# Optimization experiments

Measured on AMD Instinct MI355X. Metric: run time of the kernel, lower is better.

## Reference

```python
import jax, jax.numpy as jnp
import numpy as np

T, D = 4096, 2048
H, DK, DV = 6, 256, 512        # heads, head_k_dim, head_v_dim (expand_v=2)
KD, VD = H * DK, H * DV        # 1536, 3072
KSZ = 4                        # conv_size
GEN = D // 8                   # generator reduction 8 -> 256
EPS = 1e-5                     # norm_eps


def setup_inputs() -> dict:
    key = jax.random.key(0)
    ks = jax.random.split(key, 12)
    std = 0.02
    p = lambda i, shape: jax.random.normal(ks[i], shape, jnp.float32) * std
    rng = np.random.default_rng(0)
    A = rng.uniform(0.0, 16.0, H).astype(np.float32)
    dt = np.exp(rng.uniform(0, 1, H) * (np.log(0.1) - np.log(0.001)) + np.log(0.001)).astype(np.float32)
    dt = np.clip(dt, 1e-4, None)
    inv_dt = (dt + np.log(-np.expm1(-dt))).astype(np.float32)
    return {
        'hidden_states': jax.random.normal(ks[0], (T, D), jnp.float32),
        'Wq': p(1, (D, KD)), 'Wk': p(2, (D, KD)), 'Wv': p(3, (D, VD)),
        'Wb': p(4, (D, H)), 'Wa': p(5, (D, H)), 'Wg': p(6, (D, VD)), 'Wo': p(7, (VD, D)),
        'A_log': jnp.asarray(np.log(A)), 'dt_bias': jnp.asarray(inv_dt),
        'conv_w': p(8, (VD, KSZ)), 'gen_w1': p(9, (D, GEN)), 'gen_w2': p(10, (GEN, KSZ)),
        'norm_w': jnp.ones((DV,), jnp.float32),
    }


def _l2norm(x):
    return x * jax.lax.rsqrt(jnp.sum(x * x, -1, keepdims=True) + 1e-6)


def reference(hidden_states, Wq, Wk, Wv, Wb, Wa, Wg, Wo, A_log, dt_bias, conv_w, gen_w1, gen_w2, norm_w):
    h = hidden_states[None]                             # [1,T,D]
    q = jax.nn.silu(h @ Wq)                             # [1,T,KD]
    k = jax.nn.silu(h @ Wk)
    x = h @ Wv                                          # [1,T,VD]
    # dynamic short convolution: per-token kernel added to static depthwise kernel
    dyn = jax.nn.silu(h @ gen_w1) @ gen_w2              # [1,T,KSZ]
    xpad = jnp.pad(x, ((0, 0), (KSZ - 1, 0), (0, 0)))   # causal padding
    v = jnp.zeros_like(x)
    for j in range(KSZ):
        v = v + (conv_w[None, None, :, j] + dyn[:, :, None, j]) * xpad[:, j:j + x.shape[1], :]
    v = jax.nn.silu(v)

    B = 1
    q = _l2norm(q.reshape(B, -1, H, DK))                # use_qk_l2norm_in_kernel=True
    k = _l2norm(k.reshape(B, -1, H, DK))
    v = v.reshape(B, -1, H, DV)
    beta = jax.nn.sigmoid(h @ Wb)                       # [1,T,H]
    g = -jnp.exp(A_log) * jax.nn.softplus(h @ Wa + dt_bias)  # [1,T,H] decay log-gates
    scale = DK ** -0.5

    def step(S, inp):                                   # gated delta rule recurrence
        qt, kt, vt, gt, bt = inp
        S = S * jnp.exp(gt)[..., None, None]            # [B,H,DK,DV]
        dv = (vt - jnp.einsum('bhk,bhkv->bhv', kt, S)) * bt[..., None]
        S = S + kt[..., :, None] * dv[..., None, :]
        ot = jnp.einsum('bhk,bhkv->bhv', qt, S) * scale
        return S, ot

    S0 = jnp.zeros((B, H, DK, DV), jnp.float32)
    tm = lambda a: jnp.moveaxis(a, 1, 0)                # time-major for scan
    _, o = jax.lax.scan(step, S0, (tm(q), tm(k), tm(v), tm(g), tm(beta)))
    o = jnp.moveaxis(o, 0, 1)                           # [1,T,H,DV]

    gate = (h @ Wg).reshape(B, -1, H, DV)
    rms = jax.lax.rsqrt(jnp.mean(o * o, -1, keepdims=True) + EPS)
    o = o * rms * norm_w * jax.nn.silu(gate)            # gated RMSNorm
    o = o.reshape(B, -1, VD) @ Wo                       # [1,T,D]
    return o[0]
```

## Files before the change

kernel.cpp:

```cpp
#include <hip/hip_runtime.h>
#include <hip/hip_bf16.h>
#include <math.h>

#define T_LEN 4096
#define DIM   2048
#define NH    6
#define DK    256
#define DVh   512
#define KD    1536
#define VD    3072
#define CK    64
#define NCHK  (T_LEN / CK)
#define NFUSE 9472

typedef __attribute__((ext_vector_type(8))) short bf16x8;
typedef __attribute__((ext_vector_type(4))) float f32x4;

#define AS1 __attribute__((address_space(1)))
#define AS3 __attribute__((address_space(3)))

__device__ __forceinline__ float silu_f(float v){ return v / (1.f + __expf(-v)); }

__device__ __forceinline__ unsigned short f2bf(float f) {
  unsigned int u = __float_as_uint(f);
  unsigned int r = u + 0x7FFFu + ((u >> 16) & 1u);
  return (unsigned short)(r >> 16);
}
__device__ __forceinline__ float bf2f(unsigned short s) {
  return __uint_as_float(((unsigned int)s) << 16);
}

__device__ __forceinline__ void bar_lds() {
  __builtin_amdgcn_sched_barrier(0);
  asm volatile("s_waitcnt lgkmcnt(0)" ::: "memory");
  __builtin_amdgcn_s_barrier();
  __builtin_amdgcn_sched_barrier(0);
}

__global__ __launch_bounds__(256) void cast_bf16(
    const float* __restrict__ in, unsigned short* __restrict__ out)
{
  int i = blockIdx.x * 256 + threadIdx.x;
  float4 v4 = ((const float4*)in)[i];
  ushort4 o4;
  o4.x = f2bf(v4.x); o4.y = f2bf(v4.y); o4.z = f2bf(v4.z); o4.w = f2bf(v4.w);
  ((ushort4*)out)[i] = o4;
}

__global__ __launch_bounds__(256) void tcast_all(
    const float* __restrict__ Wq, const float* __restrict__ Wk,
    const float* __restrict__ Wv, const float* __restrict__ Wg,
    const float* __restrict__ g1, const float* __restrict__ Wo,
    unsigned short* __restrict__ wTall, unsigned short* __restrict__ wT)
{
  int id = blockIdx.x;
  const float* in; unsigned short* out; int R, Cn, nbx;
  if (id < 3072)       { in = Wq; out = wTall;                          R = 2048; Cn = 1536; nbx = 48; }
  else if (id < 6144)  { in = Wk; out = wTall + (size_t)1536 * 2048;    R = 2048; Cn = 1536; nbx = 48; id -= 3072; }
  else if (id < 12288) { in = Wv; out = wTall + (size_t)3072 * 2048;    R = 2048; Cn = 3072; nbx = 96; id -= 6144; }
  else if (id < 18432) { in = Wg; out = wTall + (size_t)6144 * 2048;    R = 2048; Cn = 3072; nbx = 96; id -= 12288; }
  else if (id < 18944) { in = g1; out = wTall + (size_t)9216 * 2048;    R = 2048; Cn = 256;  nbx = 8;  id -= 18432; }
  else                 { in = Wo; out = wT;                             R = 3072; Cn = 2048; nbx = 64; id -= 18944; }
  int bx = (id % nbx) * 32, by = (id / nbx) * 32;
  __shared__ float tile[32][33];
  int tx = threadIdx.x & 31, ty = threadIdx.x >> 5;
#pragma unroll
  for (int i = 0; i < 32; i += 8)
    tile[ty + i][tx] = in[(size_t)(by + ty + i) * Cn + bx + tx];
  __syncthreads();
#pragma unroll
  for (int i = 0; i < 32; i += 8)
    out[(size_t)(bx + ty + i) * R + by + tx] = f2bf(tile[tx][ty + i]);
}

#define PSTAGE(Amat, Bmat, bufi, t_, Aptr, Bptr, Kk) do { \
    int k0_ = (t_) << 6; \
    _Pragma("unroll") \
    for (int i_ = 0; i_ < 4; ++i_) { \
      int c_ = threadIdx.x + 256 * i_; \
      int ks_ = c_ >> 9, row_ = (c_ >> 2) & 127, pc_ = c_ & 3; \
      int pcs_ = pc_ ^ ((row_ >> 1) & 3); \
      int gc_ = k0_ + ks_ * 32 + pcs_ * 8; \
      __builtin_amdgcn_global_load_lds( \
          (const AS1 unsigned int*)(Aptr + (size_t)(bm + row_) * (Kk) + gc_), \
          (AS3 unsigned int*)(&Amat[bufi][0] + c_ * 8), 16, 0, 0); \
      __builtin_amdgcn_global_load_lds( \
          (const AS1 unsigned int*)(Bptr + (size_t)(bn + row_) * (Kk) + gc_), \
          (AS3 unsigned int*)(&Bmat[bufi][0] + c_ * 8), 16, 0, 0); \
    } } while (0)

#define PGEMM_LOOP(Amat, Bmat, Aptr, Bptr, Kk, NTt) do { \
    PSTAGE(Amat, Bmat, 0, 0, Aptr, Bptr, Kk); \
    PSTAGE(Amat, Bmat, 1, 1, Aptr, Bptr, Kk); \
    __builtin_amdgcn_sched_barrier(0); \
    asm volatile("s_waitcnt vmcnt(8)" ::: "memory"); \
    __builtin_amdgcn_s_barrier(); \
    __builtin_amdgcn_sched_barrier(0); \
    const int slot_ = (kq ^ ((fr >> 1) & 3)) * 8; \
    for (int t = 0; t < (NTt); ++t) { \
      const unsigned short* as_ = &Amat[t & 1][0]; \
      const unsigned short* bs_ = &Bmat[t & 1][0]; \
      bf16x8 af_[2][4], bf_[2][4]; \
      _Pragma("unroll") \
      for (int ks_ = 0; ks_ < 2; ++ks_) { \
        _Pragma("unroll") \
        for (int i_ = 0; i_ < 4; ++i_) { \
          af_[ks_][i_] = *(const bf16x8*)(as_ + ks_ * 4096 + (wm + i_ * 16 + fr) * 32 + slot_); \
          bf_[ks_][i_] = *(const bf16x8*)(bs_ + ks_ * 4096 + (wn + i_ * 16 + fr) * 32 + slot_); \
        } } \
      __builtin_amdgcn_s_setprio(1); \
      _Pragma("unroll") \
      for (int i_ = 0; i_ < 4; ++i_) \
        _Pragma("unroll") \
        for (int j_ = 0; j_ < 4; ++j_) \
          acc[i_][j_] = __builtin_amdgcn_mfma_f32_16x16x32_bf16(af_[0][i_], bf_[0][j_], acc[i_][j_], 0, 0, 0); \
      __builtin_amdgcn_s_setprio(0); \
      bar_lds(); \
      if (t + 2 < (NTt)) PSTAGE(Amat, Bmat, t & 1, t + 2, Aptr, Bptr, Kk); \
      __builtin_amdgcn_s_setprio(1); \
      _Pragma("unroll") \
      for (int i_ = 0; i_ < 4; ++i_) \
        _Pragma("unroll") \
        for (int j_ = 0; j_ < 4; ++j_) \
          acc[i_][j_] = __builtin_amdgcn_mfma_f32_16x16x32_bf16(af_[1][i_], bf_[1][j_], acc[i_][j_], 0, 0, 0); \
      __builtin_amdgcn_s_setprio(0); \
      __builtin_amdgcn_sched_barrier(0); \
      if (t + 2 < (NTt)) { asm volatile("s_waitcnt vmcnt(8)" ::: "memory"); } \
      else               { asm volatile("s_waitcnt vmcnt(0)" ::: "memory"); } \
      __builtin_amdgcn_s_barrier(); \
      __builtin_amdgcn_sched_barrier(0); \
    } } while (0)

__global__ __launch_bounds__(256) void gemm_bt_bf16(
    const unsigned short* __restrict__ A, const unsigned short* __restrict__ BT,
    void* __restrict__ Cout, int M, int N, int K, int act)
{
  __shared__ unsigned short As[2][8192];
  __shared__ unsigned short Bs[2][8192];
  const int tid = threadIdx.x;
  const int bm = blockIdx.y * 128, bn = blockIdx.x * 128;
  const int lane = tid & 63, wave = tid >> 6;
  const int wm = (wave >> 1) * 64, wn = (wave & 1) * 64;
  const int fr = lane & 15, kq = lane >> 4;
  const int NT = K >> 6;

  f32x4 acc[4][4];
#pragma unroll
  for (int i = 0; i < 4; ++i)
#pragma unroll
    for (int j = 0; j < 4; ++j) acc[i][j] = (f32x4){0.f, 0.f, 0.f, 0.f};

  PGEMM_LOOP(As, Bs, A, BT, K, NT);

  if (act == 2) {
    unsigned short* C = (unsigned short*)Cout;
#pragma unroll
    for (int i = 0; i < 4; ++i) {
      int rbase = bm + wm + i * 16 + kq * 4;
#pragma unroll
      for (int r = 0; r < 4; ++r) {
        size_t rowoff = (size_t)(rbase + r) * N + bn + wn + fr;
#pragma unroll
        for (int j = 0; j < 4; ++j) C[rowoff + j * 16] = f2bf(acc[i][j][r]);
      }
    }
  } else {
    float* C = (float*)Cout;
#pragma unroll
    for (int i = 0; i < 4; ++i) {
      int rbase = bm + wm + i * 16 + kq * 4;
#pragma unroll
      for (int r = 0; r < 4; ++r) {
        size_t rowoff = (size_t)(rbase + r) * N + bn + wn + fr;
#pragma unroll
        for (int j = 0; j < 4; ++j) {
          float v = acc[i][j][r];
          if (act == 1) v = silu_f(v);
          C[rowoff + j * 16] = v;
        }
      }
    }
  }
}

__global__ __launch_bounds__(256) void gemm_fused(
    const unsigned short* __restrict__ A, const unsigned short* __restrict__ BT,
    float* __restrict__ Cq, float* __restrict__ Ck, float* __restrict__ Cx,
    unsigned short* __restrict__ Cg, float* __restrict__ Ct)
{
  __shared__ unsigned short As[2][8192];
  __shared__ unsigned short Bs[2][8192];
  const int tid = threadIdx.x;
  const int NPN = NFUSE / 128;
  const int GROUP = 8;
  const int npig = GROUP * NPN;
  const int pid = blockIdx.x;
  const int gid = pid / npig;
  const int pm = gid * GROUP + (pid % GROUP);
  const int pn = (pid % npig) / GROUP;
  const int bm = pm * 128, bn = pn * 128;
  const int lane = tid & 63, wave = tid >> 6;
  const int wm = (wave >> 1) * 64, wn = (wave & 1) * 64;
  const int fr = lane & 15, kq = lane >> 4;
  const int NT = DIM >> 6;

  f32x4 acc[4][4];
#pragma unroll
  for (int i = 0; i < 4; ++i)
#pragma unroll
    for (int j = 0; j < 4; ++j) acc[i][j] = (f32x4){0.f, 0.f, 0.f, 0.f};

  PGEMM_LOOP(As, Bs, A, BT, DIM, NT);

  float* Fd = nullptr; unsigned short* Bd = nullptr;
  int strideN, cb, mode;
  if (bn < 1536)      { Fd = Cq; strideN = 1536; cb = bn;        mode = 1; }
  else if (bn < 3072) { Fd = Ck; strideN = 1536; cb = bn - 1536; mode = 1; }
  else if (bn < 6144) { Fd = Cx; strideN = 3072; cb = bn - 3072; mode = 0; }
  else if (bn < 9216) { Bd = Cg; strideN = 3072; cb = bn - 6144; mode = 2; }
  else                { Fd = Ct; strideN = 256;  cb = bn - 9216; mode = 1; }

  if (mode == 2) {
#pragma unroll
    for (int i = 0; i < 4; ++i) {
      int rbase = bm + wm + i * 16 + kq * 4;
#pragma unroll
      for (int r = 0; r < 4; ++r) {
        size_t rowoff = (size_t)(rbase + r) * strideN + cb + wn + fr;
#pragma unroll
        for (int j = 0; j < 4; ++j) Bd[rowoff + j * 16] = f2bf(acc[i][j][r]);
      }
    }
  } else {
#pragma unroll
    for (int i = 0; i < 4; ++i) {
      int rbase = bm + wm + i * 16 + kq * 4;
#pragma unroll
      for (int r = 0; r < 4; ++r) {
        size_t rowoff = (size_t)(rbase + r) * strideN + cb + wn + fr;
#pragma unroll
        for (int j = 0; j < 4; ++j) {
          float v = acc[i][j][r];
          if (mode == 1) v = silu_f(v);
          Fd[rowoff + j * 16] = v;
        }
      }
    }
  }
}

__global__ __launch_bounds__(256) void proj_dyn(
    const float* __restrict__ tg, const float* __restrict__ w2, float* __restrict__ dyn)
{
  int t = blockIdx.x, tid = threadIdx.x;
  float g = tg[(size_t)t * 256 + tid];
  float p[4];
#pragma unroll
  for (int j = 0; j < 4; ++j) p[j] = g * w2[tid * 4 + j];
#pragma unroll
  for (int j = 0; j < 4; ++j)
    for (int m = 32; m >= 1; m >>= 1) p[j] += __shfl_xor(p[j], m);
  __shared__ float red[4][4];
  if ((tid & 63) == 0) {
    int w = tid >> 6;
#pragma unroll
    for (int j = 0; j < 4; ++j) red[w][j] = p[j];
  }
  __syncthreads();
  if (tid < 4) dyn[(size_t)t * 4 + tid] = red[0][tid] + red[1][tid] + red[2][tid] + red[3][tid];
}

__global__ __launch_bounds__(256) void proj_bg(
    const float* __restrict__ h, const float* __restrict__ Wb, const float* __restrict__ Wa,
    const float* __restrict__ A_log, const float* __restrict__ dt_bias,
    float* __restrict__ beta, float* __restrict__ gout)
{
  int t = blockIdx.x, tid = threadIdx.x;
  float pb[6], pa[6];
#pragma unroll
  for (int j = 0; j < 6; ++j) { pb[j] = 0.f; pa[j] = 0.f; }
  for (int d = tid; d < DIM; d += 256) {
    float hv = h[(size_t)t * DIM + d];
#pragma unroll
    for (int j = 0; j < 6; ++j) {
      pb[j] += hv * Wb[d * 6 + j];
      pa[j] += hv * Wa[d * 6 + j];
    }
  }
#pragma unroll
  for (int j = 0; j < 6; ++j)
    for (int m = 32; m >= 1; m >>= 1) { pb[j] += __shfl_xor(pb[j], m); pa[j] += __shfl_xor(pa[j], m); }
  __shared__ float rb[4][6], ra[4][6];
  if ((tid & 63) == 0) {
    int w = tid >> 6;
#pragma unroll
    for (int j = 0; j < 6; ++j) { rb[w][j] = pb[j]; ra[w][j] = pa[j]; }
  }
  __syncthreads();
  if (tid < 6) {
    int j = tid;
    float sb = rb[0][j] + rb[1][j] + rb[2][j] + rb[3][j];
    float sa = ra[0][j] + ra[1][j] + ra[2][j] + ra[3][j];
    beta[(size_t)t * 6 + j] = 1.f / (1.f + expf(-sb));
    float z = sa + dt_bias[j];
    float sp = (z > 20.f) ? z : log1pf(expf(z));
    gout[(size_t)t * 6 + j] = -expf(A_log[j]) * sp;
  }
}

__global__ __launch_bounds__(256) void conv_kernel(
    const float* __restrict__ x, const float* __restrict__ dyn,
    const float* __restrict__ cw, float* __restrict__ v)
{
  int c = blockIdx.x * 256 + threadIdx.x;
  int t0 = blockIdx.y * 8;
  float4 w4 = ((const float4*)cw)[c];
  float xs[11];
#pragma unroll
  for (int i = 0; i < 11; ++i) {
    int t = t0 - 3 + i;
    xs[i] = (t >= 0) ? x[(size_t)t * VD + c] : 0.f;
  }
#pragma unroll
  for (int j = 0; j < 8; ++j) {
    int t = t0 + j;
    float4 dd = ((const float4*)dyn)[t];
    float acc = (w4.x + dd.x) * xs[j]
              + (w4.y + dd.y) * xs[j + 1]
              + (w4.z + dd.z) * xs[j + 2]
              + (w4.w + dd.w) * xs[j + 3];
    v[(size_t)t * VD + c] = silu_f(acc);
  }
}

__global__ __launch_bounds__(64) void cumsum_g(
    const float* __restrict__ g, float* __restrict__ c, float* __restrict__ gammas)
{
  int ch = blockIdx.x, h = blockIdx.y;
  int t0 = ch * CK;
  int lane = threadIdx.x;
  float cum = g[(size_t)(t0 + lane) * 6 + h];
  for (int off = 1; off < 64; off <<= 1) {
    float n = __shfl_up(cum, off);
    if (lane >= off) cum += n;
  }
  c[(size_t)h * T_LEN + t0 + lane] = cum;
  if (lane == 63) gammas[h * NCHK + ch] = __expf(cum);
}

__global__ __launch_bounds__(384) void l2scale(
    float* __restrict__ q, float* __restrict__ k, const float* __restrict__ c,
    unsigned short* __restrict__ Qb, unsigned short* __restrict__ Kb)
{
  int t = blockIdx.x;
  int h = threadIdx.x >> 6, lane = threadIdx.x & 63;
  size_t off = (size_t)t * KD + h * 256 + lane * 4;
  float4 qv = *(const float4*)(q + off);
  float4 kv = *(const float4*)(k + off);
  float sq = qv.x*qv.x + qv.y*qv.y + qv.z*qv.z + qv.w*qv.w;
  float sk = kv.x*kv.x + kv.y*kv.y + kv.z*kv.z + kv.w*kv.w;
  for (int m = 32; m >= 1; m >>= 1) { sq += __shfl_xor(sq, m); sk += __shfl_xor(sk, m); }
  float rq = rsqrtf(sq + 1e-6f) * 0.0625f;
  float rk = rsqrtf(sk + 1e-6f);
  qv.x *= rq; qv.y *= rq; qv.z *= rq; qv.w *= rq;
  kv.x *= rk; kv.y *= rk; kv.z *= rk; kv.w *= rk;
  *(float4*)(q + off) = qv;
  *(float4*)(k + off) = kv;
  float w1 = __expf(c[(size_t)h * T_LEN + t]);
  ushort4 qo, ko;
  qo.x = f2bf(w1 * qv.x); qo.y = f2bf(w1 * qv.y); qo.z = f2bf(w1 * qv.z); qo.w = f2bf(w1 * qv.w);
  ko.x = f2bf(w1 * kv.x); ko.y = f2bf(w1 * kv.y); ko.z = f2bf(w1 * kv.z); ko.w = f2bf(w1 * kv.w);
  *(ushort4*)(Qb + off) = qo;
  *(ushort4*)(Kb + off) = ko;
}

__global__ __launch_bounds__(256) void make_khT(
    const float* __restrict__ k, const float* __restrict__ c,
    unsigned short* __restrict__ KhT)
{
  int ch = blockIdx.x, h = blockIdx.y;
  int t0 = ch * CK;
  int tid = threadIdx.x;
  __shared__ unsigned short tile[64][258];
  __shared__ float ws[64];
  if (tid < 64) {
    float cend = c[(size_t)h * T_LEN + t0 + 63];
    ws[tid] = __expf(cend - c[(size_t)h * T_LEN + t0 + tid]);
  }
  __syncthreads();
#pragma unroll 8
  for (int rr = 0; rr < 64; ++rr) {
    float kv = k[(size_t)(t0 + rr) * KD + h * 256 + tid];
    tile[rr][tid] = f2bf(ws[rr] * kv);
  }
  __syncthreads();
  size_t obase = ((size_t)(h * NCHK + ch)) * DK * CK;
  int tt = tid & 63, kr = tid >> 6;
#pragma unroll 8
  for (int kb = 0; kb < 64; ++kb) {
    int kk = kb * 4 + kr;
    KhT[obase + (size_t)kk * CK + tt] = tile[tt][kk];
  }
}

__global__ __launch_bounds__(256) void chunk_lp(
    const float* __restrict__ q, const float* __restrict__ k,
    const float* __restrict__ c, const float* __restrict__ beta,
    float* __restrict__ Lg, unsigned short* __restrict__ Pm)
{
  const int ch = blockIdx.x, h = blockIdx.y;
  const int t0 = ch * CK;
  const int tid = threadIdx.x;
  const int w = tid >> 6, lane = tid & 63, fr = lane & 15, kq = lane >> 4;
  __shared__ unsigned short kb[64][264];
  __shared__ unsigned short qb[64][264];
  __shared__ float cs[64], bs[64];
#pragma unroll
  for (int i = 0; i < 16; ++i) {
    int fi = tid + i * 256;
    int r = fi >> 6, d4 = fi & 63;
    float4 kv = *(const float4*)(k + (size_t)(t0 + r) * KD + h * 256 + d4 * 4);
    float4 qv = *(const float4*)(q + (size_t)(t0 + r) * KD + h * 256 + d4 * 4);
    ushort4 k4, q4;
    k4.x = f2bf(kv.x); k4.y = f2bf(kv.y); k4.z = f2bf(kv.z); k4.w = f2bf(kv.w);
    q4.x = f2bf(qv.x); q4.y = f2bf(qv.y); q4.z = f2bf(qv.z); q4.w = f2bf(qv.w);
    *(ushort4*)&kb[r][d4 * 4] = k4;
    *(ushort4*)&qb[r][d4 * 4] = q4;
  }
  if (tid < 64) {
    cs[tid] = c[(size_t)h * T_LEN + t0 + tid];
    bs[tid] = beta[(size_t)(t0 + tid) * 6 + h];
  }
  __syncthreads();

  f32x4 akk[4], aqk[4];
#pragma unroll
  for (int j = 0; j < 4; ++j) { akk[j] = (f32x4){0,0,0,0}; aqk[j] = (f32x4){0,0,0,0}; }
#pragma unroll
  for (int kt = 0; kt < 8; ++kt) {
    bf16x8 ak = *(const bf16x8*)&kb[16 * w + fr][kt * 32 + kq * 8];
    bf16x8 aq = *(const bf16x8*)&qb[16 * w + fr][kt * 32 + kq * 8];
#pragma unroll
    for (int j = 0; j < 4; ++j) {
      bf16x8 b = *(const bf16x8*)&kb[j * 16 + fr][kt * 32 + kq * 8];
      akk[j] = __builtin_amdgcn_mfma_f32_16x16x32_bf16(ak, b, akk[j], 0, 0, 0);
      aqk[j] = __builtin_amdgcn_mfma_f32_16x16x32_bf16(aq, b, aqk[j], 0, 0, 0);
    }
  }
  size_t base = ((size_t)(h * NCHK + ch)) * CK * CK;
#pragma unroll
  for (int j = 0; j < 4; ++j) {
#pragma unroll
    for (int r = 0; r < 4; ++r) {
      int t = 16 * w + kq * 4 + r, col = j * 16 + fr;
      float e = __expf(fminf(cs[t] - cs[col], 0.f));
      Lg[base + t * 64 + col] = (col < t) ? bs[t] * e * akk[j][r] : 0.f;
      Pm[base + t * 64 + col] = f2bf((col <= t) ? e * aqk[j][r] : 0.f);
    }
  }
}

__global__ __launch_bounds__(64) void tri_inv(
    const float* __restrict__ Lg, const float* __restrict__ beta,
    unsigned short* __restrict__ Tm)
{
  const int ch = blockIdx.x, h = blockIdx.y;
  const size_t base = ((size_t)(h * NCHK + ch)) * CK * CK;
  const int j = threadIdx.x;
  __shared__ float Ll[64][65];
  __shared__ float Tl[64][65];
  for (int t = 0; t < 64; ++t) Ll[t][j] = Lg[base + t * 64 + j];
  __syncthreads();
  for (int t = 0; t < 64; ++t) {
    float s;
    if (j > t) s = 0.f;
    else if (j == t) s = 1.f;
    else {
      s = 0.f;
      for (int m = j; m < t; ++m) s -= Ll[t][m] * Tl[m][j];
    }
    Tl[t][j] = s;
  }
  float bj = beta[(size_t)(ch * 64 + j) * 6 + h];
  for (int t = 0; t < 64; ++t) Tm[base + t * 64 + j] = f2bf(Tl[t][j] * bj);
}

__global__ __launch_bounds__(512, 2) void scan_chunk(
    const unsigned short* __restrict__ Kb,
    const unsigned short* __restrict__ Qb,
    const unsigned short* __restrict__ KhT,
    const unsigned short* __restrict__ Tm,
    const unsigned short* __restrict__ Pm,
    const float* __restrict__ gammas,
    float* __restrict__ VO)
{
  const int h = blockIdx.y, sl = blockIdx.x;
  const int tid = threadIdx.x;
  const int w = tid >> 6, lane = tid & 63;
  const int tw = w & 3, kg = w >> 2;
  const int fr = lane & 15, kq = lane >> 4;

  __shared__ unsigned short S0h[16][264];
  __shared__ unsigned short S0l[16][264];
  __shared__ unsigned short XT[16][72];
  __shared__ unsigned short DVT[16][72];
  __shared__ float PY[2][4][16][20];
  __shared__ float PO[2][4][16][20];

  f32x4 st[2];
  st[0] = (f32x4){0.f, 0.f, 0.f, 0.f};
  st[1] = (f32x4){0.f, 0.f, 0.f, 0.f};

  const int colg = h * DVh + sl * 16 + fr;
  const size_t hc0 = (size_t)h * NCHK;

  {
    int zr = tid >> 5;
    int zc = (tid & 31) * 8;
    ushort4 z; z.x = 0; z.y = 0; z.z = 0; z.w = 0;
    *(ushort4*)&S0h[zr][zc]     = z;
    *(ushort4*)&S0h[zr][zc + 4] = z;
    *(ushort4*)&S0l[zr][zc]     = z;
    *(ushort4*)&S0l[zr][zc + 4] = z;
  }

  bf16x8 kfA[4], kfB[4], qfA[4], qfB[4];
  float vlA[4], vlB[4];

#define PREF(KF, QF, VL, chn) do { \
    const unsigned short* kr_ = Kb + (size_t)((chn) * CK + 16 * tw + fr) * KD + h * 256 + kg * 128 + kq * 8; \
    const unsigned short* qr_ = Qb + (size_t)((chn) * CK + 16 * tw + fr) * KD + h * 256 + kg * 128 + kq * 8; \
    _Pragma("unroll") \
    for (int kt = 0; kt < 4; ++kt) { \
      KF[kt] = *(const bf16x8*)(kr_ + kt * 32); \
      QF[kt] = *(const bf16x8*)(qr_ + kt * 32); } \
    if (kg == 0) { \
      _Pragma("unroll") \
      for (int r = 0; r < 4; ++r) VL[r] = VO[(size_t)((chn) * CK + 16 * tw + kq * 4 + r) * VD + colg]; } \
  } while (0)

#define BODY(chx, KF, QF, VL, KFN, QFN, VLN) do { \
    const int ch_ = (chx); \
    const int t0_ = ch_ * CK; \
    const size_t cb_ = hc0 + ch_; \
     \
    bf16x8 tpf[2]; \
    { const unsigned short* b_ = (kg == 0 ? Tm : Pm) + (cb_ * CK + 16 * tw + fr) * CK + kq * 8; \
      tpf[0] = *(const bf16x8*)(b_); tpf[1] = *(const bf16x8*)(b_ + 32); } \
    bf16x8 hfr[2][2]; \
    _Pragma("unroll") \
    for (int i = 0; i < 2; ++i) { \
      const unsigned short* hr_ = KhT + (cb_ * DK + 32 * w + 16 * i + fr) * CK + kq * 8; \
      hfr[i][0] = *(const bf16x8*)(hr_); hfr[i][1] = *(const bf16x8*)(hr_ + 32); } \
    const float gam_ = gammas[cb_]; \
    { const int chn_ = (ch_ + 1 < NCHK) ? ch_ + 1 : ch_; PREF(KFN, QFN, VLN, chn_); } \
     \
    f32x4 yt, ot; \
    { f32x4 yh = (f32x4){0.f,0.f,0.f,0.f}, yl = yh, oh = yh, ol = yh; \
      __builtin_amdgcn_s_setprio(1); \
      _Pragma("unroll") \
      for (int kt = 0; kt < 4; ++kt) { \
        const int ka_ = (kg * 4 + kt) * 32 + kq * 8; \
        bf16x8 bh_ = *(const bf16x8*)&S0h[fr][ka_]; \
        bf16x8 bl_ = *(const bf16x8*)&S0l[fr][ka_]; \
        yh = __builtin_amdgcn_mfma_f32_16x16x32_bf16(KF[kt], bh_, yh, 0, 0, 0); \
        yl = __builtin_amdgcn_mfma_f32_16x16x32_bf16(KF[kt], bl_, yl, 0, 0, 0); \
        oh = __builtin_amdgcn_mfma_f32_16x16x32_bf16(QF[kt], bh_, oh, 0, 0, 0); \
        ol = __builtin_amdgcn_mfma_f32_16x16x32_bf16(QF[kt], bl_, ol, 0, 0, 0); } \
      __builtin_amdgcn_s_setprio(0); \
      yt = yh + yl; ot = oh + ol; } \
    *(f32x4*)&PY[kg][tw][fr][kq * 4] = yt; \
    *(f32x4*)&PO[kg][tw][fr][kq * 4] = ot; \
    bar_lds();    \
    if (kg == 0) { \
      f32x4 yo = *(const f32x4*)&PY[1][tw][fr][kq * 4]; \
      ushort4 x4; \
      x4.x = f2bf(VL[0] - (yt[0] + yo[0])); \
      x4.y = f2bf(VL[1] - (yt[1] + yo[1])); \
      x4.z = f2bf(VL[2] - (yt[2] + yo[2])); \
      x4.w = f2bf(VL[3] - (yt[3] + yo[3])); \
      *(ushort4*)&XT[fr][16 * tw + kq * 4] = x4; \
    } else { \
      f32x4 oo = *(const f32x4*)&PO[0][tw][fr][kq * 4]; \
      ot[0] += oo[0]; ot[1] += oo[1]; ot[2] += oo[2]; ot[3] += oo[3]; } \
    bar_lds();    \
     \
    if (kg == 0) { \
      f32x4 d = (f32x4){0.f,0.f,0.f,0.f}; \
      bf16x8 b0_ = *(const bf16x8*)&XT[fr][kq * 8]; \
      bf16x8 b1_ = *(const bf16x8*)&XT[fr][32 + kq * 8]; \
      d = __builtin_amdgcn_mfma_f32_16x16x32_bf16(tpf[0], b0_, d, 0, 0, 0); \
      d = __builtin_amdgcn_mfma_f32_16x16x32_bf16(tpf[1], b1_, d, 0, 0, 0); \
      ushort4 d4; \
      d4.x = f2bf(d[0]); d4.y = f2bf(d[1]); d4.z = f2bf(d[2]); d4.w = f2bf(d[3]); \
      *(ushort4*)&DVT[fr][16 * tw + kq * 4] = d4; } \
    bar_lds();    \
     \
    { bf16x8 dv0_ = *(const bf16x8*)&DVT[fr][kq * 8]; \
      bf16x8 dv1_ = *(const bf16x8*)&DVT[fr][32 + kq * 8]; \
      if (kg == 1) { \
        f32x4 op = (f32x4){0.f,0.f,0.f,0.f}; \
        op = __builtin_amdgcn_mfma_f32_16x16x32_bf16(tpf[0], dv0_, op, 0, 0, 0); \
        op = __builtin_amdgcn_mfma_f32_16x16x32_bf16(tpf[1], dv1_, op, 0, 0, 0); \
        _Pragma("unroll") \
        for (int r = 0; r < 4; ++r) \
          VO[(size_t)(t0_ + 16 * tw + kq * 4 + r) * VD + colg] = ot[r] + op[r]; } \
      __builtin_amdgcn_s_setprio(1); \
      _Pragma("unroll") \
      for (int i = 0; i < 2; ++i) { \
        st[i][0] *= gam_; st[i][1] *= gam_; st[i][2] *= gam_; st[i][3] *= gam_; \
        st[i] = __builtin_amdgcn_mfma_f32_16x16x32_bf16(hfr[i][0], dv0_, st[i], 0, 0, 0); \
        st[i] = __builtin_amdgcn_mfma_f32_16x16x32_bf16(hfr[i][1], dv1_, st[i], 0, 0, 0); \
        ushort4 hi4, lo4; \
        { float s0 = st[i][0], s1 = st[i][1], s2 = st[i][2], s3 = st[i][3]; \
          hi4.x = f2bf(s0); lo4.x = f2bf(s0 - bf2f(hi4.x)); \
          hi4.y = f2bf(s1); lo4.y = f2bf(s1 - bf2f(hi4.y)); \
          hi4.z = f2bf(s2); lo4.z = f2bf(s2 - bf2f(hi4.z)); \
          hi4.w = f2bf(s3); lo4.w = f2bf(s3 - bf2f(hi4.w)); } \
        *(ushort4*)&S0h[fr][32 * w + 16 * i + kq * 4] = hi4; \
        *(ushort4*)&S0l[fr][32 * w + 16 * i + kq * 4] = lo4; } \
      __builtin_amdgcn_s_setprio(0); } \
    bar_lds();    \
  } while (0)

  PREF(kfA, qfA, vlA, 0);
  __syncthreads();
  for (int ch = 0; ch < NCHK; ch += 2) {
    BODY(ch,     kfA, qfA, vlA, kfB, qfB, vlB);
    BODY(ch + 1, kfB, qfB, vlB, kfA, qfA, vlA);
  }
#undef BODY
#undef PREF
}

__global__ __launch_bounds__(256) void norm_gate(
    const float* __restrict__ o, const unsigned short* __restrict__ gate,
    const float* __restrict__ nw, unsigned short* __restrict__ out)
{
  int th = blockIdx.x, tid = threadIdx.x;
  size_t base = (size_t)th * DVh;
  float x0 = o[base + tid], x1 = o[base + 256 + tid];
  float ss = x0 * x0 + x1 * x1;
  for (int m = 32; m >= 1; m >>= 1) ss += __shfl_xor(ss, m);
  __shared__ float red[4];
  if ((tid & 63) == 0) red[tid >> 6] = ss;
  __syncthreads();
  float rms = rsqrtf((red[0] + red[1] + red[2] + red[3]) * (1.f / 512.f) + 1e-5f);
  float g0 = bf2f(gate[base + tid]), g1 = bf2f(gate[base + 256 + tid]);
  out[base + tid]       = f2bf(x0 * rms * nw[tid]       * silu_f(g0));
  out[base + 256 + tid] = f2bf(x1 * rms * nw[tid + 256] * silu_f(g1));
}

extern "C" void kernel_launch(void* const* d_in, const int* in_sizes, int n_in,
                              void* d_out, int out_size, void* d_ws, size_t ws_size,
                              hipStream_t stream)
{
  const float* h       = (const float*)d_in[0];
  const float* Wq      = (const float*)d_in[1];
  const float* Wk      = (const float*)d_in[2];
  const float* Wv      = (const float*)d_in[3];
  const float* Wb      = (const float*)d_in[4];
  const float* Wa      = (const float*)d_in[5];
  const float* Wg      = (const float*)d_in[6];
  const float* Wo      = (const float*)d_in[7];
  const float* A_log   = (const float*)d_in[8];
  const float* dt_bias = (const float*)d_in[9];
  const float* conv_w  = (const float*)d_in[10];
  const float* gen_w1  = (const float*)d_in[11];
  const float* gen_w2  = (const float*)d_in[12];
  const float* norm_w  = (const float*)d_in[13];
  float* out = (float*)d_out;

  const size_t TK = (size_t)T_LEN * KD, TV = (size_t)T_LEN * VD, TD = (size_t)T_LEN * DIM;

  float* ws   = (float*)d_ws;
  float* q    = ws;
  float* k    = q    + TK;
  float* x    = k    + TK;
  float* v    = x    + TV;
  float* tg   = v    + TV;
  float* dyn  = tg   + (size_t)T_LEN * 256;
  float* beta = dyn  + (size_t)T_LEN * 4;
  float* g    = beta + (size_t)T_LEN * 6;
  float* c    = g    + (size_t)T_LEN * 6;
  float* gam  = c    + (size_t)NH * T_LEN;
  float* fend = gam  + 512;
  unsigned short* bh      = (unsigned short*)fend;
  unsigned short* wT      = bh      + TD;
  unsigned short* gate_bf = wT      + (size_t)DIM * VD;
  unsigned short* go_bf   = gate_bf + TV;
  unsigned short* Kb_s  = bh;
  unsigned short* Qb_s  = (unsigned short*)x;
  unsigned short* KhT_s = Qb_s + TK;
  unsigned short* Tm_s  = KhT_s + TK;
  unsigned short* Pm_s  = Tm_s + (size_t)NH * NCHK * CK * CK;
  float* Lg = (float*)go_bf;
  unsigned short* wTall = (unsigned short*)v;

  dim3 blk(256);
  cast_bf16<<<(TD / 4) / 256, blk, 0, stream>>>(h, bh);
  tcast_all<<<25088, blk, 0, stream>>>(Wq, Wk, Wv, Wg, gen_w1, Wo, wTall, wT);
  gemm_fused<<<dim3((NFUSE / 128) * (T_LEN / 128)), blk, 0, stream>>>(
      bh, wTall, q, k, x, gate_bf, tg);

  proj_bg<<<T_LEN, blk, 0, stream>>>(h, Wb, Wa, A_log, dt_bias, beta, g);
  cumsum_g<<<dim3(NCHK, NH), 64, 0, stream>>>(g, c, gam);
  proj_dyn<<<T_LEN, blk, 0, stream>>>(tg, gen_w2, dyn);
  conv_kernel<<<dim3(VD / 256, T_LEN / 8), blk, 0, stream>>>(x, dyn, conv_w, v);
  l2scale<<<T_LEN, 384, 0, stream>>>(q, k, c, Qb_s, Kb_s);

  make_khT<<<dim3(NCHK, NH), blk, 0, stream>>>(k, c, KhT_s);
  chunk_lp<<<dim3(NCHK, NH), blk, 0, stream>>>(q, k, c, beta, Lg, Pm_s);
  tri_inv<<<dim3(NCHK, NH), 64, 0, stream>>>(Lg, beta, Tm_s);

  scan_chunk<<<dim3(DVh / 16, NH), 512, 0, stream>>>(Kb_s, Qb_s, KhT_s, Tm_s, Pm_s, gam, v);

  norm_gate<<<T_LEN * NH, blk, 0, stream>>>(v, gate_bf, norm_w, go_bf);
  gemm_bt_bf16<<<dim3(DIM / 128, T_LEN / 128), blk, 0, stream>>>(go_bf, wT, out, T_LEN, DIM, VD, 0);
}
```

Measured before the change: 896.2 us.

## Fuse bf16 cast with beta/gate projection and merge chunk prep kernels

Merges the bf16 cast of hidden states with the beta/decay-gate projection so h is read once, removing the separate proj_bg launch. Also fuses make_khT, chunk_lp and tri_inv into one kernel that builds KhT and keeps the L matrix in LDS for the triangular inversion, avoiding the Lg global round trip and two launches. The cost is that tri_inv now runs on only 64 threads inside a 256-thread block. The KhT writes are uncoalesced in the new layout, and reusing the LDS buffers adds extra barriers.

```diff
diff --git a/kernel.cpp b/kernel.cpp
--- a/kernel.cpp
+++ b/kernel.cpp
@@ -37,14 +37,52 @@
   __builtin_amdgcn_sched_barrier(0);
 }
 
-__global__ __launch_bounds__(256) void cast_bf16(
-    const float* __restrict__ in, unsigned short* __restrict__ out)
-{
-  int i = blockIdx.x * 256 + threadIdx.x;
-  float4 v4 = ((const float4*)in)[i];
-  ushort4 o4;
-  o4.x = f2bf(v4.x); o4.y = f2bf(v4.y); o4.z = f2bf(v4.z); o4.w = f2bf(v4.w);
-  ((ushort4*)out)[i] = o4;
+__global__ __launch_bounds__(256) void cast_bg(
+    const float* __restrict__ h, const float* __restrict__ Wb, const float* __restrict__ Wa,
+    const float* __restrict__ A_log, const float* __restrict__ dt_bias,
+    unsigned short* __restrict__ bh, float* __restrict__ beta, float* __restrict__ gout)
+{
+  int t = blockIdx.x, tid = threadIdx.x;
+  size_t base = (size_t)t * DIM + tid * 8;
+  float4 h0 = *(const float4*)(h + base);
+  float4 h1 = *(const float4*)(h + base + 4);
+  ushort4 o0, o1;
+  o0.x = f2bf(h0.x); o0.y = f2bf(h0.y); o0.z = f2bf(h0.z); o0.w = f2bf(h0.w);
+  o1.x = f2bf(h1.x); o1.y = f2bf(h1.y); o1.z = f2bf(h1.z); o1.w = f2bf(h1.w);
+  *(ushort4*)(bh + base)     = o0;
+  *(ushort4*)(bh + base + 4) = o1;
+  float hv[8] = {h0.x, h0.y, h0.z, h0.w, h1.x, h1.y, h1.z, h1.w};
+  float pb[6], pa[6];
+#pragma unroll
+  for (int j = 0; j < 6; ++j) { pb[j] = 0.f; pa[j] = 0.f; }
+  const float* wbp = Wb + (size_t)(tid * 8) * 6;
+  const float* wap = Wa + (size_t)(tid * 8) * 6;
+#pragma unroll
+  for (int i = 0; i < 8; ++i)
+#pragma unroll
+    for (int j = 0; j < 6; ++j) {
+      pb[j] += hv[i] * wbp[i * 6 + j];
+      pa[j] += hv[i] * wap[i * 6 + j];
+    }
+#pragma unroll
+  for (int j = 0; j < 6; ++j)
+    for (int m = 32; m >= 1; m >>= 1) { pb[j] += __shfl_xor(pb[j], m); pa[j] += __shfl_xor(pa[j], m); }
+  __shared__ float rb[4][6], ra[4][6];
+  if ((tid & 63) == 0) {
+    int w = tid >> 6;
+#pragma unroll
+    for (int j = 0; j < 6; ++j) { rb[w][j] = pb[j]; ra[w][j] = pa[j]; }
+  }
+  __syncthreads();
+  if (tid < 6) {
+    int j = tid;
+    float sb = rb[0][j] + rb[1][j] + rb[2][j] + rb[3][j];
+    float sa = ra[0][j] + ra[1][j] + ra[2][j] + ra[3][j];
+    beta[(size_t)t * 6 + j] = 1.f / (1.f + expf(-sb));
+    float z = sa + dt_bias[j];
+    float sp = (z > 20.f) ? z : log1pf(expf(z));
+    gout[(size_t)t * 6 + j] = -expf(A_log[j]) * sp;
+  }
 }
 
 __global__ __launch_bounds__(256) void tcast_all(
@@ -270,44 +308,6 @@
   if (tid < 4) dyn[(size_t)t * 4 + tid] = red[0][tid] + red[1][tid] + red[2][tid] + red[3][tid];
 }
 
-__global__ __launch_bounds__(256) void proj_bg(
-    const float* __restrict__ h, const float* __restrict__ Wb, const float* __restrict__ Wa,
-    const float* __restrict__ A_log, const float* __restrict__ dt_bias,
-    float* __restrict__ beta, float* __restrict__ gout)
-{
-  int t = blockIdx.x, tid = threadIdx.x;
-  float pb[6], pa[6];
-#pragma unroll
-  for (int j = 0; j < 6; ++j) { pb[j] = 0.f; pa[j] = 0.f; }
-  for (int d = tid; d < DIM; d += 256) {
-    float hv = h[(size_t)t * DIM + d];
-#pragma unroll
-    for (int j = 0; j < 6; ++j) {
-      pb[j] += hv * Wb[d * 6 + j];
-      pa[j] += hv * Wa[d * 6 + j];
-    }
-  }
-#pragma unroll
-  for (int j = 0; j < 6; ++j)
-    for (int m = 32; m >= 1; m >>= 1) { pb[j] += __shfl_xor(pb[j], m); pa[j] += __shfl_xor(pa[j], m); }
-  __shared__ float rb[4][6], ra[4][6];
-  if ((tid & 63) == 0) {
-    int w = tid >> 6;
-#pragma unroll
-    for (int j = 0; j < 6; ++j) { rb[w][j] = pb[j]; ra[w][j] = pa[j]; }
-  }
-  __syncthreads();
-  if (tid < 6) {
-    int j = tid;
-    float sb = rb[0][j] + rb[1][j] + rb[2][j] + rb[3][j];
-    float sa = ra[0][j] + ra[1][j] + ra[2][j] + ra[3][j];
-    beta[(size_t)t * 6 + j] = 1.f / (1.f + expf(-sb));
-    float z = sa + dt_bias[j];
-    float sp = (z > 20.f) ? z : log1pf(expf(z));
-    gout[(size_t)t * 6 + j] = -expf(A_log[j]) * sp;
-  }
-}
-
 __global__ __launch_bounds__(256) void conv_kernel(
     const float* __restrict__ x, const float* __restrict__ dyn,
     const float* __restrict__ cw, float* __restrict__ v)
@@ -374,39 +374,11 @@
   *(ushort4*)(Kb + off) = ko;
 }
 
-__global__ __launch_bounds__(256) void make_khT(
-    const float* __restrict__ k, const float* __restrict__ c,
-    unsigned short* __restrict__ KhT)
-{
-  int ch = blockIdx.x, h = blockIdx.y;
-  int t0 = ch * CK;
-  int tid = threadIdx.x;
-  __shared__ unsigned short tile[64][258];
-  __shared__ float ws[64];
-  if (tid < 64) {
-    float cend = c[(size_t)h * T_LEN + t0 + 63];
-    ws[tid] = __expf(cend - c[(size_t)h * T_LEN + t0 + tid]);
-  }
-  __syncthreads();
-#pragma unroll 8
-  for (int rr = 0; rr < 64; ++rr) {
-    float kv = k[(size_t)(t0 + rr) * KD + h * 256 + tid];
-    tile[rr][tid] = f2bf(ws[rr] * kv);
-  }
-  __syncthreads();
-  size_t obase = ((size_t)(h * NCHK + ch)) * DK * CK;
-  int tt = tid & 63, kr = tid >> 6;
-#pragma unroll 8
-  for (int kb = 0; kb < 64; ++kb) {
-    int kk = kb * 4 + kr;
-    KhT[obase + (size_t)kk * CK + tt] = tile[tt][kk];
-  }
-}
-
-__global__ __launch_bounds__(256) void chunk_lp(
+__global__ __launch_bounds__(256) void lp_fused(
     const float* __restrict__ q, const float* __restrict__ k,
     const float* __restrict__ c, const float* __restrict__ beta,
-    float* __restrict__ Lg, unsigned short* __restrict__ Pm)
+    unsigned short* __restrict__ Pm, unsigned short* __restrict__ Tm,
+    unsigned short* __restrict__ KhT)
 {
   const int ch = blockIdx.x, h = blockIdx.y;
   const int t0 = ch * CK;
@@ -415,6 +387,8 @@
   __shared__ unsigned short kb[64][264];
   __shared__ unsigned short qb[64][264];
   __shared__ float cs[64], bs[64];
+  float (*Ll)[65] = (float (*)[65])kb;
+  float (*Tl)[65] = (float (*)[65])qb;
 #pragma unroll
   for (int i = 0; i < 16; ++i) {
     int fi = tid + i * 256;
@@ -433,6 +407,18 @@
   }
   __syncthreads();
 
+  {
+    int tt = tid & 63, ks = tid >> 6;
+    float w2 = __expf(cs[63] - cs[tt]);
+    size_t obase = ((size_t)(h * NCHK + ch)) * DK * CK;
+#pragma unroll 8
+    for (int kb2 = 0; kb2 < 64; ++kb2) {
+      int kk = ks * 64 + kb2;
+      float kv = k[(size_t)(t0 + tt) * KD + h * 256 + kk];
+      KhT[obase + (size_t)kk * CK + tt] = f2bf(w2 * kv);
+    }
+  }
+
   f32x4 akk[4], aqk[4];
 #pragma unroll
   for (int j = 0; j < 4; ++j) { akk[j] = (f32x4){0,0,0,0}; aqk[j] = (f32x4){0,0,0,0}; }
@@ -447,6 +433,8 @@
       aqk[j] = __builtin_amdgcn_mfma_f32_16x16x32_bf16(aq, b, aqk[j], 0, 0, 0);
     }
   }
+  __syncthreads();
+
   size_t base = ((size_t)(h * NCHK + ch)) * CK * CK;
 #pragma unroll
   for (int j = 0; j < 4; ++j) {
@@ -454,35 +442,27 @@
     for (int r = 0; r < 4; ++r) {
       int t = 16 * w + kq * 4 + r, col = j * 16 + fr;
       float e = __expf(fminf(cs[t] - cs[col], 0.f));
-      Lg[base + t * 64 + col] = (col < t) ? bs[t] * e * akk[j][r] : 0.f;
+      Ll[t][col] = (col < t) ? bs[t] * e * akk[j][r] : 0.f;
       Pm[base + t * 64 + col] = f2bf((col <= t) ? e * aqk[j][r] : 0.f);
     }
   }
-}
-
-__global__ __launch_bounds__(64) void tri_inv(
-    const float* __restrict__ Lg, const float* __restrict__ beta,
-    unsigned short* __restrict__ Tm)
-{
-  const int ch = blockIdx.x, h = blockIdx.y;
-  const size_t base = ((size_t)(h * NCHK + ch)) * CK * CK;
-  const int j = threadIdx.x;
-  __shared__ float Ll[64][65];
-  __shared__ float Tl[64][65];
-  for (int t = 0; t < 64; ++t) Ll[t][j] = Lg[base + t * 64 + j];
-  __syncthreads();
-  for (int t = 0; t < 64; ++t) {
-    float s;
-    if (j > t) s = 0.f;
-    else if (j == t) s = 1.f;
-    else {
-      s = 0.f;
-      for (int m = j; m < t; ++m) s -= Ll[t][m] * Tl[m][j];
-    }
-    Tl[t][j] = s;
-  }
-  float bj = beta[(size_t)(ch * 64 + j) * 6 + h];
-  for (int t = 0; t < 64; ++t) Tm[base + t * 64 + j] = f2bf(Tl[t][j] * bj);
+  __syncthreads();
+
+  if (tid < 64) {
+    int j = tid;
+    for (int t = 0; t < 64; ++t) {
+      float s;
+      if (j > t) s = 0.f;
+      else if (j == t) s = 1.f;
+      else {
+        s = 0.f;
+        for (int m = j; m < t; ++m) s -= Ll[t][m] * Tl[m][j];
+      }
+      Tl[t][j] = s;
+    }
+    float bj = bs[j];
+    for (int t = 0; t < 64; ++t) Tm[base + t * 64 + j] = f2bf(Tl[t][j] * bj);
+  }
 }
 
 __global__ __launch_bounds__(512, 2) void scan_chunk(
@@ -694,24 +674,20 @@
   unsigned short* KhT_s = Qb_s + TK;
   unsigned short* Tm_s  = KhT_s + TK;
   unsigned short* Pm_s  = Tm_s + (size_t)NH * NCHK * CK * CK;
-  float* Lg = (float*)go_bf;
   unsigned short* wTall = (unsigned short*)v;
 
   dim3 blk(256);
-  cast_bf16<<<(TD / 4) / 256, blk, 0, stream>>>(h, bh);
+  cast_bg<<<T_LEN, blk, 0, stream>>>(h, Wb, Wa, A_log, dt_bias, bh, beta, g);
   tcast_all<<<25088, blk, 0, stream>>>(Wq, Wk, Wv, Wg, gen_w1, Wo, wTall, wT);
   gemm_fused<<<dim3((NFUSE / 128) * (T_LEN / 128)), blk, 0, stream>>>(
       bh, wTall, q, k, x, gate_bf, tg);
 
-  proj_bg<<<T_LEN, blk, 0, stream>>>(h, Wb, Wa, A_log, dt_bias, beta, g);
   cumsum_g<<<dim3(NCHK, NH), 64, 0, stream>>>(g, c, gam);
   proj_dyn<<<T_LEN, blk, 0, stream>>>(tg, gen_w2, dyn);
   conv_kernel<<<dim3(VD / 256, T_LEN / 8), blk, 0, stream>>>(x, dyn, conv_w, v);
   l2scale<<<T_LEN, 384, 0, stream>>>(q, k, c, Qb_s, Kb_s);
 
-  make_khT<<<dim3(NCHK, NH), blk, 0, stream>>>(k, c, KhT_s);
-  chunk_lp<<<dim3(NCHK, NH), blk, 0, stream>>>(q, k, c, beta, Lg, Pm_s);
-  tri_inv<<<dim3(NCHK, NH), 64, 0, stream>>>(Lg, beta, Tm_s);
+  lp_fused<<<dim3(NCHK, NH), blk, 0, stream>>>(q, k, c, beta, Pm_s, Tm_s, KhT_s);
 
   scan_chunk<<<dim3(DVh / 16, NH), 512, 0, stream>>>(Kb_s, Qb_s, KhT_s, Tm_s, Pm_s, gam, v);
 
```

Result: no change. 908.4 us (+1.4%).
